# Optimization experiments

Measured on AMD Instinct MI355X. Metric: run time of the kernel, lower is better.

Reference implementation:

```python
import jax, jax.numpy as jnp
import numpy as np

TP, TQ, B, I, H = 400, 60, 16, 256, 256  # passage len, question len, batch, input, hidden (I == H so 2*I == 2*H)


def setup_inputs() -> dict:
    key = jax.random.key(0)
    ks = jax.random.split(key, 10)
    g = lambda k, sh, sc: jax.random.normal(k, sh, dtype=jnp.float32) * sc
    return dict(
        passage_repr=g(ks[0], (TP, B, I), 1.0),
        question_repr=g(ks[1], (TQ, B, I), 1.0),
        passage_mask=jnp.ones((TP, B), jnp.float32),
        question_mask=jnp.ones((TQ, B), jnp.float32),
        WuQ=g(ks[2], (H, I), 0.05),            # nn.Linear(input, hidden, bias=False)
        WuP=g(ks[3], (H, I), 0.05),
        v=g(ks[4], (H,), 0.05),                # vT: nn.Linear(hidden, 1, bias=False)
        Wg=g(ks[5], (2 * I, 2 * I), 0.02),     # gate linear
        gru_Wih=g(ks[6], (3, 2, 3 * H, 2 * H), 0.05),  # [layer, dir, 3H, in] (in = 2*I = 2*H)
        gru_Whh=g(ks[7], (3, 2, 3 * H, H), 0.05),
        gru_bih=g(ks[8], (3, 2, 3 * H), 0.02),
        gru_bhh=g(ks[9], (3, 2, 3 * H), 0.02),
    )


def _gru_dir(x, Wih, Whh, bih, bhh, reverse):
    # x: [T, B, in] -> ys: [T, B, H]; PyTorch GRU gate order (r, z, n)
    xg = jnp.einsum('tbi,gi->tbg', x, Wih) + bih  # precompute input gates [T,B,3H]
    if reverse:
        xg = xg[::-1]
    Hh = Whh.shape[1]

    def step(h, xt):
        gh = h @ Whh.T + bhh
        xr, xz, xn = jnp.split(xt, 3, axis=-1)
        hr, hz, hn = jnp.split(gh, 3, axis=-1)
        r = jax.nn.sigmoid(xr + hr)
        z = jax.nn.sigmoid(xz + hz)
        n = jnp.tanh(xn + r * hn)
        h = (1.0 - z) * n + z * h
        return h, h

    h0 = jnp.zeros((x.shape[1], Hh), x.dtype)
    _, ys = jax.lax.scan(step, h0, xg)
    return ys[::-1] if reverse else ys


def _forward(passage_repr, question_repr, question_mask, WuQ, WuP, v, Wg,
             gru_Wih, gru_Whh, gru_bih, gru_bhh):
    Qh = question_repr @ WuQ.T                 # [Tq,B,H]
    Ph = passage_repr @ WuP.T                  # [Tp,B,H]
    # additive attention score s[q,p,b] = v . tanh(Qh[q,b] + Ph[p,b])
    scores = jnp.tanh(Qh[:, None] + Ph[None]) @ v   # [Tq,Tp,B]
    m = question_mask[:, None, :]              # [Tq,1,B]
    logits = m * scores + (1.0 - m) * (-1e30)  # masked_softmax over question dim
    a = jax.nn.softmax(logits, axis=0)         # [Tq,Tp,B]
    ct = jnp.einsum('qpb,qbi->pbi', a, question_repr)      # attended question [Tp,B,I]
    ct = jnp.concatenate([passage_repr, ct], axis=-1)       # [Tp,B,2I]
    x = ct * jax.nn.sigmoid(ct @ Wg.T)                      # gated input
    for layer in range(3):                                  # 3-layer bidirectional GRU (eval: no dropout)
        f = _gru_dir(x, gru_Wih[layer, 0], gru_Whh[layer, 0], gru_bih[layer, 0], gru_bhh[layer, 0], False)
        b = _gru_dir(x, gru_Wih[layer, 1], gru_Whh[layer, 1], gru_bih[layer, 1], gru_bhh[layer, 1], True)
        x = jnp.concatenate([f, b], axis=-1)                # [Tp,B,2H]
    return x


def reference(passage_repr, question_repr, passage_mask, question_mask, WuQ, WuP, v, Wg,
              gru_Wih, gru_Whh, gru_bih, gru_bhh):
    # passage_mask is accepted (as in the original forward) but unused
    return _forward(passage_repr, question_repr, question_mask, WuQ, WuP, v, Wg,
                    gru_Wih, gru_Whh, gru_bih, gru_bhh)
```

## Files before the change

kernel.cpp:

```cpp
#include <hip/hip_runtime.h>
#include <math.h>

#define TPQ 60
#define TPP 400
#define BB  16
#define II  256
#define HH  256

typedef short bf16x8 __attribute__((ext_vector_type(8)));
typedef float f32x4  __attribute__((ext_vector_type(4)));
typedef unsigned short u16;

__device__ __forceinline__ float sigm(float x){ return 1.0f/(1.0f+__expf(-x)); }
__device__ __forceinline__ float tanhfast(float x){
  x = fminf(fmaxf(x,-20.0f),20.0f);
  float t = __expf(2.0f*x);
  return (t-1.0f)/(t+1.0f);
}
__device__ __forceinline__ short f2bf(float f){
  unsigned u = __float_as_uint(f);
  unsigned r = (u + 0x7fffu + ((u>>16)&1u)) >> 16;
  return (short)r;
}
__device__ __forceinline__ float bf2f(short h){
  return __uint_as_float(((unsigned)(unsigned short)h)<<16);
}

__global__ void transpose_k(float* __restrict__ dst, const float* __restrict__ src,
                            int R, int C, int dstStride, int dstOff){
  int idx = blockIdx.x*256 + threadIdx.x;
  if (idx >= R*C) return;
  int r = idx / C, c = idx % C;
  dst[(size_t)c*dstStride + dstOff + r] = src[idx];
}

__global__ void f2bf_k(const float* __restrict__ src, u16* __restrict__ dst, int n){
  int i = blockIdx.x*256 + threadIdx.x;
  if (i < n) dst[i] = (u16)f2bf(src[i]);
}

template<int EP>
__global__ __launch_bounds__(256) void gemm_f32(const float* __restrict__ A, const float* __restrict__ B,
    const float* __restrict__ bias, const float* __restrict__ msrc, float* __restrict__ C,
    int M, int N, int K)
{
  __shared__ float As[8][128];
  __shared__ float Bs[8][128];
  int tid = threadIdx.x;
  int m0 = blockIdx.y*128, n0 = blockIdx.x*128;
  int tx = tid & 15, ty = tid >> 4;
  float acc[8][8];
  #pragma unroll
  for (int i=0;i<8;i++)
    #pragma unroll
    for (int j=0;j<8;j++) acc[i][j] = 0.0f;

  int arow = tid >> 1, ak = (tid & 1)*4;
  int brow = tid >> 5, bcol = (tid & 31)*4;

  for (int k0=0;k0<K;k0+=8){
    float4 av;
    if (m0 + arow < M) av = *reinterpret_cast<const float4*>(&A[(size_t)(m0+arow)*K + k0 + ak]);
    else { av.x=0; av.y=0; av.z=0; av.w=0; }
    As[ak+0][arow]=av.x; As[ak+1][arow]=av.y; As[ak+2][arow]=av.z; As[ak+3][arow]=av.w;
    float4 bv = *reinterpret_cast<const float4*>(&B[(size_t)(k0+brow)*N + n0 + bcol]);
    *reinterpret_cast<float4*>(&Bs[brow][bcol]) = bv;
    __syncthreads();
    #pragma unroll
    for (int k=0;k<8;k++){
      float a[8], bb[8];
      *reinterpret_cast<float4*>(&a[0]) = *reinterpret_cast<const float4*>(&As[k][ty*8]);
      *reinterpret_cast<float4*>(&a[4]) = *reinterpret_cast<const float4*>(&As[k][ty*8+4]);
      *reinterpret_cast<float4*>(&bb[0]) = *reinterpret_cast<const float4*>(&Bs[k][tx*8]);
      *reinterpret_cast<float4*>(&bb[4]) = *reinterpret_cast<const float4*>(&Bs[k][tx*8+4]);
      #pragma unroll
      for (int i=0;i<8;i++)
        #pragma unroll
        for (int j=0;j<8;j++) acc[i][j] += a[i]*bb[j];
    }
    __syncthreads();
  }
  #pragma unroll
  for (int i=0;i<8;i++){
    int m = m0 + ty*8 + i;
    if (m >= M) continue;
    #pragma unroll
    for (int j=0;j<8;j++){
      int n = n0 + tx*8 + j;
      float val = acc[i][j];
      if (bias) val += bias[n];
      if (EP==1) val = msrc[(size_t)m*N + n] * sigm(val);
      C[(size_t)m*N + n] = val;
    }
  }
}

template<int EP>
__global__ __launch_bounds__(256) void gemm_bf16_hl(
    const float* __restrict__ Af,
    const u16* __restrict__ Wb,
    const float* __restrict__ bias,
    const float* __restrict__ msrc,
    float* __restrict__ C, int M, int N, int K)
{
  __shared__ u16 sAh[4096], sAl[4096], sW[4096];
  const int tid = threadIdx.x;
  const int lane = tid & 63, wv = tid >> 6;
  const int nl = lane & 15, kq = lane >> 4;
  const int m0 = blockIdx.y*128, n0 = blockIdx.x*128;
  const int wm16 = (wv>>1)*4, wn16 = (wv&1)*4;

  f32x4 acc[4][4];
  #pragma unroll
  for (int mi=0;mi<4;mi++)
    #pragma unroll
    for (int ni=0;ni<4;ni++) acc[mi][ni] = (f32x4){0.f,0.f,0.f,0.f};

  for (int k0=0; k0<K; k0+=32){
    #pragma unroll
    for (int it=0; it<2; it++){
      int c = tid + it*256;
      int row = c >> 2, q = c & 3;
      int ldsoff = ((row>>4)*64 + q*16 + (row&15))*8;
      bf16x8 h = (bf16x8){0,0,0,0,0,0,0,0}, l = (bf16x8){0,0,0,0,0,0,0,0};
      if (m0 + row < M){
        size_t ga = (size_t)(m0+row)*K + k0 + q*8;
        float4 a0 = *reinterpret_cast<const float4*>(&Af[ga]);
        float4 a1 = *reinterpret_cast<const float4*>(&Af[ga+4]);
        float av[8] = {a0.x,a0.y,a0.z,a0.w,a1.x,a1.y,a1.z,a1.w};
        #pragma unroll
        for (int e=0;e<8;e++){
          short hb = f2bf(av[e]);
          h[e] = hb;
          l[e] = f2bf(av[e] - bf2f(hb));
        }
      }
      *reinterpret_cast<bf16x8*>(&sAh[ldsoff]) = h;
      *reinterpret_cast<bf16x8*>(&sAl[ldsoff]) = l;
      size_t gw = (size_t)(n0+row)*K + k0 + q*8;
      *reinterpret_cast<uint4*>(&sW[ldsoff]) = *reinterpret_cast<const uint4*>(&Wb[gw]);
    }
    __syncthreads();
    bf16x8 ah[4], al[4], wr[4];
    #pragma unroll
    for (int mi=0;mi<4;mi++){
      int off = ((wm16+mi)*64 + kq*16 + nl)*8;
      ah[mi] = *reinterpret_cast<const bf16x8*>(&sAh[off]);
      al[mi] = *reinterpret_cast<const bf16x8*>(&sAl[off]);
    }
    #pragma unroll
    for (int ni=0;ni<4;ni++){
      int off = ((wn16+ni)*64 + kq*16 + nl)*8;
      wr[ni] = *reinterpret_cast<const bf16x8*>(&sW[off]);
    }
    #pragma unroll
    for (int mi=0;mi<4;mi++)
      #pragma unroll
      for (int ni=0;ni<4;ni++){
        acc[mi][ni] = __builtin_amdgcn_mfma_f32_16x16x32_bf16(ah[mi], wr[ni], acc[mi][ni], 0, 0, 0);
        acc[mi][ni] = __builtin_amdgcn_mfma_f32_16x16x32_bf16(al[mi], wr[ni], acc[mi][ni], 0, 0, 0);
      }
    __syncthreads();
  }
  #pragma unroll
  for (int mi=0;mi<4;mi++){
    #pragma unroll
    for (int ni=0;ni<4;ni++){
      int col = n0 + (wn16+ni)*16 + nl;
      float bv = bias ? bias[col] : 0.0f;
      #pragma unroll
      for (int r2=0;r2<4;r2++){
        int rrow = m0 + (wm16+mi)*16 + kq*4 + r2;
        if (rrow >= M) continue;
        float val = acc[mi][ni][r2] + bv;
        if (EP==1) val = msrc[(size_t)rrow*N + col] * sigm(val);
        C[(size_t)rrow*N + col] = val;
      }
    }
  }
}

__global__ __launch_bounds__(256) void attn_k(const float* __restrict__ Qh, const float* __restrict__ Ph,
   const float* __restrict__ qrep, const float* __restrict__ prep, const float* __restrict__ v,
   const float* __restrict__ qmask, float* __restrict__ xcat)
{
  int p = blockIdx.x, b = blockIdx.y;
  int tid = threadIdx.x;
  __shared__ float ph[HH];
  __shared__ float vv[HH];
  __shared__ float sc[64];
  size_t pb = (size_t)p*BB + b;
  ph[tid] = Ph[pb*HH + tid];
  vv[tid] = v[tid];
  xcat[pb*512 + tid] = prep[pb*II + tid];
  __syncthreads();
  int wid = tid >> 6, lane = tid & 63;
  for (int q = wid; q < TPQ; q += 4){
    const float* qh = Qh + ((size_t)q*BB + b)*HH;
    float s = 0.0f;
    for (int hh = lane; hh < HH; hh += 64)
      s += vv[hh]*tanhfast(qh[hh] + ph[hh]);
    #pragma unroll
    for (int off=32; off>0; off>>=1) s += __shfl_xor(s, off);
    if (lane==0) sc[q] = s;
  }
  __syncthreads();
  if (wid==0){
    float m = (lane < TPQ) ? qmask[lane*BB + b] : 0.0f;
    float val = (lane < TPQ) ? (m*sc[lane] + (1.0f-m)*(-1e30f)) : -INFINITY;
    float mx = val;
    #pragma unroll
    for (int off=32; off>0; off>>=1) mx = fmaxf(mx, __shfl_xor(mx, off));
    float e = (lane < TPQ) ? __expf(val - mx) : 0.0f;
    float sum = e;
    #pragma unroll
    for (int off=32; off>0; off>>=1) sum += __shfl_xor(sum, off);
    if (lane < TPQ) sc[lane] = e / sum;
  }
  __syncthreads();
  float acc = 0.0f;
  for (int q=0;q<TPQ;q++)
    acc += sc[q] * qrep[((size_t)q*BB + b)*II + tid];
  xcat[pb*512 + 256 + tid] = acc;
}

__global__ __launch_bounds__(512) void gru_scan_mfma(
    const float* __restrict__ xg,
    const float* __restrict__ Whh,
    const float* __restrict__ bhh,
    float* __restrict__ out)
{
  __shared__ u16 hbuf[2][256];

  const int b   = blockIdx.x & 15;
  const int dir = blockIdx.x >> 4;
  const int tid  = threadIdx.x;
  const int wv   = tid >> 6;
  const int lane = tid & 63;
  const int nl   = lane & 15;
  const int kq   = lane >> 4;

  ((u16*)hbuf)[tid] = 0;

  bf16x8 wreg[8][6];
  #pragma unroll
  for (int ks=0; ks<8; ks++){
    #pragma unroll
    for (int gg=0; gg<2; gg++){
      #pragma unroll
      for (int gi=0; gi<3; gi++){
        int nrow = gi*256 + wv*32 + gg*16 + nl;
        const float* wsrc = Whh + (size_t)dir*768*256 + (size_t)nrow*256 + ks*32 + kq*8;
        float4 lo = *reinterpret_cast<const float4*>(wsrc);
        float4 hi = *reinterpret_cast<const float4*>(wsrc+4);
        bf16x8 f;
        f[0]=f2bf(lo.x); f[1]=f2bf(lo.y); f[2]=f2bf(lo.z); f[3]=f2bf(lo.w);
        f[4]=f2bf(hi.x); f[5]=f2bf(hi.y); f[6]=f2bf(hi.z); f[7]=f2bf(hi.w);
        wreg[ks][gg*3+gi] = f;
      }
    }
  }

  float bias[2][3];
  #pragma unroll
  for (int gg=0; gg<2; gg++)
    #pragma unroll
    for (int gi=0; gi<3; gi++)
      bias[gg][gi] = bhh[dir*768 + gi*256 + wv*32 + gg*16 + nl];

  const float* xb = xg + dir*768 + wv*32 + nl;

  float hold[2] = {0.0f, 0.0f};

  __syncthreads();

  #pragma unroll 1
  for (int s=0; s<TPP; s++){
    const int t = dir ? (TPP-1-s) : s;

    float xv[2][3];
    {
      size_t ro = (size_t)(t*16 + b)*1536;
      #pragma unroll
      for (int gg=0; gg<2; gg++)
        #pragma unroll
        for (int gi=0; gi<3; gi++)
          xv[gg][gi] = xb[ro + gi*256 + gg*16];
    }

    f32x4 acc[2][3];
    #pragma unroll
    for (int gg=0; gg<2; gg++)
      #pragma unroll
      for (int gi=0; gi<3; gi++)
        acc[gg][gi] = (f32x4){0.f,0.f,0.f,0.f};

    const char* hp = (const char*)hbuf[s&1];
    bf16x8 a = *reinterpret_cast<const bf16x8*>(hp + kq*16);
    #pragma unroll
    for (int ks=0; ks<8; ks++){
      bf16x8 an;
      if (ks < 7)
        an = *reinterpret_cast<const bf16x8*>(hp + (ks+1)*64 + kq*16);
      #pragma unroll
      for (int gg=0; gg<2; gg++)
        #pragma unroll
        for (int gi=0; gi<3; gi++)
          acc[gg][gi] = __builtin_amdgcn_mfma_f32_16x16x32_bf16(a, wreg[ks][gg*3+gi], acc[gg][gi], 0, 0, 0);
      if (ks < 7) a = an;
    }

    if (lane < 16){
      u16* wb = hbuf[(s&1)^1];
      #pragma unroll
      for (int gg=0; gg<2; gg++){
        int j = wv*32 + gg*16 + nl;
        float r = sigm(xv[gg][0] + acc[gg][0][0] + bias[gg][0]);
        float z = sigm(xv[gg][1] + acc[gg][1][0] + bias[gg][1]);
        float n = tanhfast(xv[gg][2] + r*(acc[gg][2][0] + bias[gg][2]));
        float hv = (1.0f - z)*n + z*hold[gg];
        hold[gg] = hv;
        wb[j] = (u16)f2bf(hv);
        out[(size_t)(t*16 + b)*512 + dir*256 + j] = hv;
      }
    }
    __syncthreads();
  }
}

extern "C" void kernel_launch(void* const* d_in, const int* in_sizes, int n_in,
                              void* d_out, int out_size, void* d_ws, size_t ws_size,
                              hipStream_t stream)
{
  const float* prep  = (const float*)d_in[0];
  const float* qrep  = (const float*)d_in[1];
  const float* qmask = (const float*)d_in[3];
  const float* WuQ   = (const float*)d_in[4];
  const float* WuP   = (const float*)d_in[5];
  const float* v     = (const float*)d_in[6];
  const float* Wg    = (const float*)d_in[7];
  const float* Wih   = (const float*)d_in[8];
  const float* Whh   = (const float*)d_in[9];
  const float* bih   = (const float*)d_in[10];
  const float* bhh   = (const float*)d_in[11];
  float* out = (float*)d_out;

  float* ws = (float*)d_ws;
  size_t off = 0;
  float* WuQT = ws + off; off += 256*256;
  float* WuPT = ws + off; off += 256*256;
  float* Qh   = ws + off; off += (size_t)TPQ*BB*HH;
  float* Ph   = ws + off; off += (size_t)TPP*BB*HH;
  float* xcat = ws + off; off += (size_t)TPP*BB*512;
  float* ybuf = ws + off; off += (size_t)TPP*BB*512;
  float* xg   = ws + off; off += (size_t)TPP*BB*1536;
  u16*  Wb    = (u16*)(ws + off); off += (size_t)3*1536*512/2;
  u16*  Wgb   = (u16*)(ws + off); off += (size_t)512*512/2;

  auto T = [&](float* dst, const float* src, int R, int C, int st, int o){
    int n = R*C;
    transpose_k<<<dim3((n+255)/256), dim3(256), 0, stream>>>(dst, src, R, C, st, o);
  };
  T(WuQT, WuQ, 256,256,256,0);
  T(WuPT, WuP, 256,256,256,0);
  {
    int n = 3*1536*512;
    f2bf_k<<<dim3((n+255)/256), dim3(256), 0, stream>>>(Wih, Wb, n);
    n = 512*512;
    f2bf_k<<<dim3((n+255)/256), dim3(256), 0, stream>>>(Wg, Wgb, n);
  }

  gemm_f32<0><<<dim3(2, 8), dim3(256), 0, stream>>>(qrep, WuQT, nullptr, nullptr, Qh, TPQ*BB, 256, 256);
  gemm_f32<0><<<dim3(2, 50), dim3(256), 0, stream>>>(prep, WuPT, nullptr, nullptr, Ph, TPP*BB, 256, 256);
  attn_k<<<dim3(TPP, BB), dim3(256), 0, stream>>>(Qh, Ph, qrep, prep, v, qmask, xcat);
  gemm_bf16_hl<1><<<dim3(4, 50), dim3(256), 0, stream>>>(xcat, Wgb, nullptr, xcat, ybuf, TPP*BB, 512, 512);

  float* cur = ybuf;
  float* nxt = xcat;
  for (int l=0;l<3;l++){
    gemm_bf16_hl<0><<<dim3(12, 50), dim3(256), 0, stream>>>(cur, Wb + (size_t)l*1536*512,
                                                            bih + (size_t)l*1536, nullptr, xg, TPP*BB, 1536, 512);
    float* o = (l==2) ? out : nxt;
    gru_scan_mfma<<<dim3(32), dim3(512), 0, stream>>>(xg, Whh + (size_t)l*2*768*256,
                                                      bhh + (size_t)l*2*768, o);
    float* tmp = cur; cur = o; nxt = tmp;
  }
}
```

Baseline: 2.310 ms.

## Use bf16 MFMA GEMMs for projections and streamline GRU scan loop

Replaces the FP32 SIMT GEMMs and transposes for the Q/P projections with the existing bf16 hi/lo MFMA GEMM, which consumes the weights directly after bf16 conversion. The GRU scan is unrolled by two with separate ping-pong LDS buffers and pointer-stepping for input and output addresses. The hidden bias is folded into the accumulator initialisation. The GRU scan dominates runtime, so the projection change mostly trims small kernels. The scan changes cut per-step index arithmetic on the serial critical path.

```diff
diff --git a/kernel.cpp b/kernel.cpp
--- a/kernel.cpp
+++ b/kernel.cpp
@@ -26,73 +26,9 @@
   return __uint_as_float(((unsigned)(unsigned short)h)<<16);
 }
 
-__global__ void transpose_k(float* __restrict__ dst, const float* __restrict__ src,
-                            int R, int C, int dstStride, int dstOff){
-  int idx = blockIdx.x*256 + threadIdx.x;
-  if (idx >= R*C) return;
-  int r = idx / C, c = idx % C;
-  dst[(size_t)c*dstStride + dstOff + r] = src[idx];
-}
-
 __global__ void f2bf_k(const float* __restrict__ src, u16* __restrict__ dst, int n){
   int i = blockIdx.x*256 + threadIdx.x;
   if (i < n) dst[i] = (u16)f2bf(src[i]);
-}
-
-template<int EP>
-__global__ __launch_bounds__(256) void gemm_f32(const float* __restrict__ A, const float* __restrict__ B,
-    const float* __restrict__ bias, const float* __restrict__ msrc, float* __restrict__ C,
-    int M, int N, int K)
-{
-  __shared__ float As[8][128];
-  __shared__ float Bs[8][128];
-  int tid = threadIdx.x;
-  int m0 = blockIdx.y*128, n0 = blockIdx.x*128;
-  int tx = tid & 15, ty = tid >> 4;
-  float acc[8][8];
-  #pragma unroll
-  for (int i=0;i<8;i++)
-    #pragma unroll
-    for (int j=0;j<8;j++) acc[i][j] = 0.0f;
-
-  int arow = tid >> 1, ak = (tid & 1)*4;
-  int brow = tid >> 5, bcol = (tid & 31)*4;
-
-  for (int k0=0;k0<K;k0+=8){
-    float4 av;
-    if (m0 + arow < M) av = *reinterpret_cast<const float4*>(&A[(size_t)(m0+arow)*K + k0 + ak]);
-    else { av.x=0; av.y=0; av.z=0; av.w=0; }
-    As[ak+0][arow]=av.x; As[ak+1][arow]=av.y; As[ak+2][arow]=av.z; As[ak+3][arow]=av.w;
-    float4 bv = *reinterpret_cast<const float4*>(&B[(size_t)(k0+brow)*N + n0 + bcol]);
-    *reinterpret_cast<float4*>(&Bs[brow][bcol]) = bv;
-    __syncthreads();
-    #pragma unroll
-    for (int k=0;k<8;k++){
-      float a[8], bb[8];
-      *reinterpret_cast<float4*>(&a[0]) = *reinterpret_cast<const float4*>(&As[k][ty*8]);
-      *reinterpret_cast<float4*>(&a[4]) = *reinterpret_cast<const float4*>(&As[k][ty*8+4]);
-      *reinterpret_cast<float4*>(&bb[0]) = *reinterpret_cast<const float4*>(&Bs[k][tx*8]);
-      *reinterpret_cast<float4*>(&bb[4]) = *reinterpret_cast<const float4*>(&Bs[k][tx*8+4]);
-      #pragma unroll
-      for (int i=0;i<8;i++)
-        #pragma unroll
-        for (int j=0;j<8;j++) acc[i][j] += a[i]*bb[j];
-    }
-    __syncthreads();
-  }
-  #pragma unroll
-  for (int i=0;i<8;i++){
-    int m = m0 + ty*8 + i;
-    if (m >= M) continue;
-    #pragma unroll
-    for (int j=0;j<8;j++){
-      int n = n0 + tx*8 + j;
-      float val = acc[i][j];
-      if (bias) val += bias[n];
-      if (EP==1) val = msrc[(size_t)m*N + n] * sigm(val);
-      C[(size_t)m*N + n] = val;
-    }
-  }
 }
 
 template<int EP>
@@ -230,7 +166,8 @@
     const float* __restrict__ bhh,
     float* __restrict__ out)
 {
-  __shared__ u16 hbuf[2][256];
+  __shared__ u16 hbuf0[256];
+  __shared__ u16 hbuf1[256];
 
   const int b   = blockIdx.x & 15;
   const int dir = blockIdx.x >> 4;
@@ -240,7 +177,7 @@
   const int nl   = lane & 15;
   const int kq   = lane >> 4;
 
-  ((u16*)hbuf)[tid] = 0;
+  if (tid < 256) hbuf0[tid] = 0;
 
   bf16x8 wreg[8][6];
   #pragma unroll
@@ -268,34 +205,34 @@
     for (int gi=0; gi<3; gi++)
       bias[gg][gi] = bhh[dir*768 + gi*256 + wv*32 + gg*16 + nl];
 
-  const float* xb = xg + dir*768 + wv*32 + nl;
+  const int t0  = dir ? (TPP-1) : 0;
+  const ptrdiff_t xstride = (dir ? -1 : 1) * (ptrdiff_t)(16*1536);
+  const ptrdiff_t ostride = (dir ? -1 : 1) * (ptrdiff_t)(16*512);
+  const float* xp = xg + (size_t)(t0*16 + b)*1536 + dir*768 + wv*32 + nl;
+  float* op = out + (size_t)(t0*16 + b)*512 + dir*256 + wv*32 + nl;
 
   float hold[2] = {0.0f, 0.0f};
 
   __syncthreads();
 
-  #pragma unroll 1
-  for (int s=0; s<TPP; s++){
-    const int t = dir ? (TPP-1-s) : s;
-
+  auto body = [&](const u16* __restrict__ rb, u16* __restrict__ wb){
     float xv[2][3];
-    {
-      size_t ro = (size_t)(t*16 + b)*1536;
-      #pragma unroll
-      for (int gg=0; gg<2; gg++)
-        #pragma unroll
-        for (int gi=0; gi<3; gi++)
-          xv[gg][gi] = xb[ro + gi*256 + gg*16];
-    }
+    #pragma unroll
+    for (int gg=0; gg<2; gg++)
+      #pragma unroll
+      for (int gi=0; gi<3; gi++)
+        xv[gg][gi] = xp[gi*256 + gg*16];
 
     f32x4 acc[2][3];
     #pragma unroll
     for (int gg=0; gg<2; gg++)
       #pragma unroll
-      for (int gi=0; gi<3; gi++)
-        acc[gg][gi] = (f32x4){0.f,0.f,0.f,0.f};
-
-    const char* hp = (const char*)hbuf[s&1];
+      for (int gi=0; gi<3; gi++){
+        float bv = bias[gg][gi];
+        acc[gg][gi] = (f32x4){bv,bv,bv,bv};
+      }
+
+    const char* hp = (const char*)rb;
     bf16x8 a = *reinterpret_cast<const bf16x8*>(hp + kq*16);
     #pragma unroll
     for (int ks=0; ks<8; ks++){
@@ -311,20 +248,26 @@
     }
 
     if (lane < 16){
-      u16* wb = hbuf[(s&1)^1];
       #pragma unroll
       for (int gg=0; gg<2; gg++){
         int j = wv*32 + gg*16 + nl;
-        float r = sigm(xv[gg][0] + acc[gg][0][0] + bias[gg][0]);
-        float z = sigm(xv[gg][1] + acc[gg][1][0] + bias[gg][1]);
-        float n = tanhfast(xv[gg][2] + r*(acc[gg][2][0] + bias[gg][2]));
+        float r = sigm(xv[gg][0] + acc[gg][0][0]);
+        float z = sigm(xv[gg][1] + acc[gg][1][0]);
+        float n = tanhfast(xv[gg][2] + r*acc[gg][2][0]);
         float hv = (1.0f - z)*n + z*hold[gg];
         hold[gg] = hv;
         wb[j] = (u16)f2bf(hv);
-        out[(size_t)(t*16 + b)*512 + dir*256 + j] = hv;
-      }
-    }
+        op[gg*16] = hv;
+      }
+    }
+    xp += xstride; op += ostride;
     __syncthreads();
+  };
+
+  #pragma unroll 1
+  for (int s=0; s<TPP; s+=2){
+    body(hbuf0, hbuf1);
+    body(hbuf1, hbuf0);
   }
 }
 
@@ -347,8 +290,6 @@
 
   float* ws = (float*)d_ws;
   size_t off = 0;
-  float* WuQT = ws + off; off += 256*256;
-  float* WuPT = ws + off; off += 256*256;
   float* Qh   = ws + off; off += (size_t)TPQ*BB*HH;
   float* Ph   = ws + off; off += (size_t)TPP*BB*HH;
   float* xcat = ws + off; off += (size_t)TPP*BB*512;
@@ -356,22 +297,21 @@
   float* xg   = ws + off; off += (size_t)TPP*BB*1536;
   u16*  Wb    = (u16*)(ws + off); off += (size_t)3*1536*512/2;
   u16*  Wgb   = (u16*)(ws + off); off += (size_t)512*512/2;
-
-  auto T = [&](float* dst, const float* src, int R, int C, int st, int o){
-    int n = R*C;
-    transpose_k<<<dim3((n+255)/256), dim3(256), 0, stream>>>(dst, src, R, C, st, o);
-  };
-  T(WuQT, WuQ, 256,256,256,0);
-  T(WuPT, WuP, 256,256,256,0);
+  u16*  Wqb   = (u16*)(ws + off); off += (size_t)256*256/2;
+  u16*  Wpb   = (u16*)(ws + off); off += (size_t)256*256/2;
+
   {
     int n = 3*1536*512;
     f2bf_k<<<dim3((n+255)/256), dim3(256), 0, stream>>>(Wih, Wb, n);
     n = 512*512;
     f2bf_k<<<dim3((n+255)/256), dim3(256), 0, stream>>>(Wg, Wgb, n);
-  }
-
-  gemm_f32<0><<<dim3(2, 8), dim3(256), 0, stream>>>(qrep, WuQT, nullptr, nullptr, Qh, TPQ*BB, 256, 256);
-  gemm_f32<0><<<dim3(2, 50), dim3(256), 0, stream>>>(prep, WuPT, nullptr, nullptr, Ph, TPP*BB, 256, 256);
+    n = 256*256;
+    f2bf_k<<<dim3((n+255)/256), dim3(256), 0, stream>>>(WuQ, Wqb, n);
+    f2bf_k<<<dim3((n+255)/256), dim3(256), 0, stream>>>(WuP, Wpb, n);
+  }
+
+  gemm_bf16_hl<0><<<dim3(2, 8), dim3(256), 0, stream>>>(qrep, Wqb, nullptr, nullptr, Qh, TPQ*BB, 256, 256);
+  gemm_bf16_hl<0><<<dim3(2, 50), dim3(256), 0, stream>>>(prep, Wpb, nullptr, nullptr, Ph, TPP*BB, 256, 256);
   attn_k<<<dim3(TPP, BB), dim3(256), 0, stream>>>(Qh, Ph, qrep, prep, v, qmask, xcat);
   gemm_bf16_hl<1><<<dim3(4, 50), dim3(256), 0, stream>>>(xcat, Wgb, nullptr, xcat, ybuf, TPP*BB, 512, 512);
 
```

New measurement: 3.315 ms. 1.43x slower.
